# Optimization experiments

Hardware: AMD Instinct MI355X
Metric: run time of the kernel (lower is better)

Reference implementation:

```python
import jax, jax.numpy as jnp
import numpy as np

B, T, N, H, MAX_LAG = 16, 28, 2048, 32, 7
LN_EPS = 1e-5


def setup_inputs() -> dict:
    key = jax.random.key(0)
    ks = jax.random.split(key, 10)
    s = 1.0 / np.sqrt(H)  # nn.Linear-like init scale
    x = jax.random.uniform(ks[0], (B, T, N), dtype=jnp.float32)
    features = jax.random.normal(ks[1], (B, N, H), dtype=jnp.float32)
    # delay logits init: log(softmax-able exp(-tau/3) normalized + 1e-8)
    w = np.exp(-np.arange(MAX_LAG + 1, dtype=np.float32) / 3.0)
    w = w / w.sum()
    delay_logits = jnp.log(jnp.asarray(w, dtype=jnp.float32) + 1e-8)
    Wq = jax.random.normal(ks[2], (H, H), dtype=jnp.float32) * s
    Wk = jax.random.normal(ks[3], (H, H), dtype=jnp.float32) * s
    Wv = jax.random.normal(ks[4], (H, H), dtype=jnp.float32) * s
    Wo = jax.random.normal(ks[5], (H, H), dtype=jnp.float32) * s
    bq = jnp.zeros((H,), jnp.float32)
    bk = jnp.zeros((H,), jnp.float32)
    bv = jnp.zeros((H,), jnp.float32)
    bo = jnp.zeros((H,), jnp.float32)
    adj = jax.random.uniform(ks[6], (N, N), dtype=jnp.float32)
    adj_prior = adj / (adj.sum(axis=-1, keepdims=True) + 1e-8)  # row-normalized
    geo_weight = jnp.float32(0.3)
    gamma = jnp.ones((H,), jnp.float32)
    beta = jnp.zeros((H,), jnp.float32)
    return {"x": x, "features": features, "delay_logits": delay_logits,
            "Wq": Wq, "bq": bq, "Wk": Wk, "bk": bk, "Wv": Wv, "bv": bv,
            "adj_prior": adj_prior, "geo_weight": geo_weight,
            "Wo": Wo, "bo": bo, "gamma": gamma, "beta": beta}


def reference(x, features, delay_logits, Wq, bq, Wk, bk, Wv, bv,
              adj_prior, geo_weight, Wo, bo, gamma, beta):
    L = MAX_LAG + 1  # number of delay taps (T >= L here)
    delay_w = jax.nn.softmax(delay_logits, axis=0)  # [L]
    # delayed signal: sum_tau w[tau] * x[:, -(tau+1), :]
    lagged = x[:, -L:, :][:, ::-1, :]               # [B, L, N], tau-th row = x[:, -(tau+1)]
    delayed_signal = jnp.einsum('t,btn->bn', delay_w, lagged)  # [B, N]

    Q = features @ Wq.T + bq                        # [B, N, H]
    K = features @ Wk.T + bk
    V = features @ Wv.T + bv
    scores = jnp.einsum('bnh,bmh->bnm', Q, K) / np.sqrt(H).astype(np.float32)
    geo = jax.nn.sigmoid(geo_weight)
    scores = (1.0 - geo) * scores + geo * adj_prior[None, :, :] * 5.0
    attn = jax.nn.softmax(scores, axis=-1)          # [B, N, N]

    propagated = jnp.einsum('bnm,bm->bn', attn, delayed_signal)  # [B, N]
    attended = jnp.einsum('bnm,bmh->bnh', attn, V)               # [B, N, H]
    combined = features + attended + propagated[..., None] * 0.1

    h = combined @ Wo.T + bo
    mu = h.mean(axis=-1, keepdims=True)
    var = ((h - mu) ** 2).mean(axis=-1, keepdims=True)
    out = (h - mu) * jax.lax.rsqrt(var + LN_EPS) * gamma + beta
    return out
```

## Files before the change

kernel.cpp:

```cpp
#include <hip/hip_runtime.h>
#include <hip/hip_bf16.h>
#include <math.h>
#include <stdint.h>

#define Bb 16
#define Tt 28
#define Nn 2048
#define Hh 32
#define LAGS 8
#define LN_EPS 1e-5f
#define PSTR 56

typedef float f4 __attribute__((ext_vector_type(4)));
typedef short s8v __attribute__((ext_vector_type(8)));
typedef unsigned short u16x4 __attribute__((ext_vector_type(4)));
typedef unsigned short u16x8 __attribute__((ext_vector_type(8)));

__device__ __forceinline__ float b2f(unsigned short u) {
    union { unsigned uu; float ff; } x; x.uu = ((unsigned)u) << 16; return x.ff;
}
__device__ __forceinline__ unsigned short f2b(float f) {
    unsigned u = __float_as_uint(f);
    u += 0x7FFFu + ((u >> 16) & 1u);
    return (unsigned short)(u >> 16);
}
__device__ __forceinline__ unsigned packbf2(float lo, float hi) {
    __hip_bfloat162 h = __float22bfloat162_rn(make_float2(lo, hi));
    union { __hip_bfloat162 h2; unsigned u; } c; c.h2 = h; return c.u;
}

__global__ void k_adjprep(const float* __restrict__ adj, const float* __restrict__ geo_w,
                          unsigned short* __restrict__ adjF) {
    __shared__ float T[16][516];
    float geo = 1.f / (1.f + __expf(-geo_w[0]));
    float cg = geo * 5.f;
    int tid = threadIdx.x;
    int g = blockIdx.x >> 2, q = blockIdx.x & 3;
    int n0 = g * 16, m0 = q * 512;
    #pragma unroll
    for (int r = 0; r < 16; ++r) {
        T[r][tid] = adj[(size_t)(n0 + r) * Nn + m0 + tid];
        T[r][tid + 256] = adj[(size_t)(n0 + r) * Nn + m0 + tid + 256];
    }
    __syncthreads();
    unsigned short* region = adjF + ((size_t)g * 512 + q * 128) * 64;
    #pragma unroll
    for (int i = 0; i < 4; ++i) {
        int e0 = (i * 256 + tid) * 8;
        u16x8 w;
        #pragma unroll
        for (int j = 0; j < 8; ++j) {
            int e = e0 + j;
            int mq = e >> 6, nl = (e >> 2) & 15, mm = e & 3;
            w[j] = f2b(cg * T[nl][mq * 4 + mm]);
        }
        *(u16x8*)(region + e0) = w;
    }
}

__global__ void k_qkv(const float* __restrict__ feat, const float* __restrict__ x,
                      const float* __restrict__ dlog,
                      const float* __restrict__ Wq, const float* __restrict__ bq,
                      const float* __restrict__ Wk, const float* __restrict__ bk,
                      const float* __restrict__ Wv, const float* __restrict__ bv,
                      const float* __restrict__ geo_w,
                      unsigned short* __restrict__ Qbf, unsigned short* __restrict__ Kf,
                      unsigned short* __restrict__ Vf) {
    __shared__ float WqT[Hh][Hh + 1], WkT[Hh][Hh + 1], WvT[Hh][Hh + 1];
    __shared__ float f[8][Hh];
    __shared__ __align__(16) unsigned short VT8[Hh][8];
    __shared__ __align__(16) unsigned short DS8[8];
    int tid = threadIdx.x;
    for (int i = tid; i < Hh * Hh; i += 256) {
        int h = i >> 5, k = i & 31;
        WqT[k][h] = Wq[i];
        WkT[k][h] = Wk[i];
        WvT[k][h] = Wv[i];
    }
    int n0 = blockIdx.x * 8;
    int b = n0 >> 11, mloc0 = n0 & 2047;
    if (tid < 64) {
        float mx = -1e30f;
        #pragma unroll
        for (int t = 0; t < LAGS; ++t) mx = fmaxf(mx, dlog[t]);
        float s = 0.f, wv[LAGS];
        #pragma unroll
        for (int t = 0; t < LAGS; ++t) { wv[t] = __expf(dlog[t] - mx); s += wv[t]; }
        int t = tid >> 3, j = tid & 7;
        float dsv = (wv[t] / s) * x[(size_t)b * Tt * Nn + (size_t)(Tt - 1 - t) * Nn + mloc0 + j];
        dsv += __shfl_xor(dsv, 8);
        dsv += __shfl_xor(dsv, 16);
        dsv += __shfl_xor(dsv, 32);
        if (tid < 8) DS8[tid] = f2b(dsv);
    }
    float geo = 1.f / (1.f + __expf(-geo_w[0]));
    float cs = (1.f - geo) * 0.17677669529663687f;
    f[tid >> 5][tid & 31] = feat[(size_t)n0 * Hh + tid];
    __syncthreads();
    int lr = tid >> 5, h = tid & 31;
    float aq = bq[h], ak = bk[h], av = bv[h];
    #pragma unroll
    for (int k = 0; k < Hh; ++k) {
        float fv = f[lr][k];
        aq += fv * WqT[k][h];
        ak += fv * WkT[k][h];
        av += fv * WvT[k][h];
    }
    Qbf[(size_t)(n0 + lr) * Hh + h] = f2b(aq * cs);
    int mloc = mloc0 + lr;
    size_t kaddr = ((((size_t)b * 128 + (mloc >> 4)) * 4 + (h >> 3)) * 16 + (mloc & 15)) * 8 + (h & 7);
    Kf[kaddr] = f2b(ak);
    VT8[h][lr] = f2b(av);
    __syncthreads();
    size_t vbase = (((size_t)b * 64 + (mloc0 >> 5)) * 4 + ((mloc0 >> 3) & 3)) * 48;
    if (tid < 32) {
        *(u16x8*)(Vf + (vbase + tid) * 8) = *(const u16x8*)&VT8[tid][0];
    } else if (tid < 48) {
        int rr = tid - 32;
        u16x8 wv8;
        if (rr == 0) {
            wv8 = *(const u16x8*)&DS8[0];
        } else {
            unsigned short fill = (rr == 1) ? (unsigned short)0x3F80 : (unsigned short)0;
            for (int j = 0; j < 8; ++j) wv8[j] = fill;
        }
        *(u16x8*)(Vf + (vbase + 32 + rr) * 8) = wv8;
    }
}

__global__ __launch_bounds__(256, 2)
void k_attn(const unsigned short* __restrict__ Qbf,
            const unsigned short* __restrict__ Kf,
            const unsigned short* __restrict__ Vf,
            const unsigned short* __restrict__ adjF,
            const float* __restrict__ feat,
            const float* __restrict__ Wo, const float* __restrict__ bo,
            const float* __restrict__ gamma, const float* __restrict__ beta,
            float* __restrict__ out) {
    __shared__ __align__(16) unsigned short Pt[4][32 * PSTR];
    __shared__ float WoT[Hh][Hh + 1];
    __shared__ float combT[32][Hh + 1];
    __shared__ float gbb[3][Hh];

    int tid = threadIdx.x;
    int wid = tid >> 6, lane = tid & 63;
    int nl = lane & 15, g4 = lane >> 4;
    int wh = wid;

    for (int i = tid; i < Hh * Hh; i += 256) WoT[i & 31][i >> 5] = Wo[i];
    if (tid < 32) { gbb[0][tid] = bo[tid]; gbb[1][tid] = gamma[tid]; gbb[2][tid] = beta[tid]; }

    int bid = blockIdx.x;
    int xcd = bid & 7, r = bid >> 3;
    int b = ((xcd & 1) << 3) + (r & 7);
    int nt32 = ((xcd >> 1) << 4) + (r >> 3);
    int n0w = nt32 * 32;

    s8v qf[2];
    #pragma unroll
    for (int nt = 0; nt < 2; ++nt)
        qf[nt] = *(const s8v*)(Qbf + (((size_t)b * Nn + n0w + nt * 16 + nl) << 5) + g4 * 8);

    f4 pacc[2][3];
    #pragma unroll
    for (int nt = 0; nt < 2; ++nt)
        #pragma unroll
        for (int t = 0; t < 3; ++t) pacc[nt][t] = (f4){0.f, 0.f, 0.f, 0.f};

    const unsigned short* Kb = Kf + (size_t)b * 65536;
    const unsigned short* Vb = Vf + (size_t)b * 98304;
    unsigned short* Pw = Pt[wid];

    const unsigned short* pK  = Kb + (((size_t)(wh * 2) * 4 + g4) * 16 + nl) * 8;
    const unsigned short* pV  = Vb + (((size_t)wh * 4 + g4) * 48 + nl) * 8;
    const unsigned short* pA0 = adjF + ((size_t)(nt32 * 2) * 512 + wh * 8 + g4) * 64 + nl * 4;
    const unsigned short* pA1 = adjF + ((size_t)(nt32 * 2 + 1) * 512 + wh * 8 + g4) * 64 + nl * 4;

    struct Frag {
        s8v kf0, kf1, vf0, vf1, vf2;
        u16x4 a00, a01, a10, a11;
    };

    auto loadP = [&](Frag& F) {
        F.kf0 = *(const s8v*)(pK);
        F.kf1 = *(const s8v*)(pK + 512);
        F.vf0 = *(const s8v*)(pV);
        F.vf1 = *(const s8v*)(pV + 128);
        F.vf2 = *(const s8v*)(pV + 256);
        F.a00 = *(const u16x4*)(pA0);
        F.a01 = *(const u16x4*)(pA0 + 256);
        F.a10 = *(const u16x4*)(pA1);
        F.a11 = *(const u16x4*)(pA1 + 256);
        pK += 4096;
        pV += 6144;
        pA0 += 2048;
        pA1 += 2048;
    };

    auto mkC = [&](u16x4 av) -> f4 {
        f4 C;
        C[0] = b2f(av[0]); C[1] = b2f(av[1]); C[2] = b2f(av[2]); C[3] = b2f(av[3]);
        return C;
    };

    auto SM = [&](f4 sc, int nt, int mg) {
        float p0 = __expf(sc[0]), p1 = __expf(sc[1]);
        float p2 = __expf(sc[2]), p3 = __expf(sc[3]);
        uint2 w;
        w.x = packbf2(p0, p1);
        w.y = packbf2(p2, p3);
        *(uint2*)(Pw + (size_t)(nt * 16 + nl) * PSTR + mg * 16 + g4 * 4) = w;
    };

    auto compute = [&](Frag& F) {
        f4 sc00 = __builtin_amdgcn_mfma_f32_16x16x32_bf16(F.kf0, qf[0], mkC(F.a00), 0, 0, 0);
        f4 sc01 = __builtin_amdgcn_mfma_f32_16x16x32_bf16(F.kf1, qf[0], mkC(F.a01), 0, 0, 0);
        f4 sc10 = __builtin_amdgcn_mfma_f32_16x16x32_bf16(F.kf0, qf[1], mkC(F.a10), 0, 0, 0);
        f4 sc11 = __builtin_amdgcn_mfma_f32_16x16x32_bf16(F.kf1, qf[1], mkC(F.a11), 0, 0, 0);
        SM(sc00, 0, 0);
        SM(sc01, 0, 1);
        SM(sc10, 1, 0);
        SM(sc11, 1, 1);
        s8v pb0 = *(const s8v*)(Pw + (size_t)(0 * 16 + nl) * PSTR + g4 * 8);
        s8v pb1 = *(const s8v*)(Pw + (size_t)(1 * 16 + nl) * PSTR + g4 * 8);
        pacc[0][0] = __builtin_amdgcn_mfma_f32_16x16x32_bf16(F.vf0, pb0, pacc[0][0], 0, 0, 0);
        pacc[0][1] = __builtin_amdgcn_mfma_f32_16x16x32_bf16(F.vf1, pb0, pacc[0][1], 0, 0, 0);
        pacc[0][2] = __builtin_amdgcn_mfma_f32_16x16x32_bf16(F.vf2, pb0, pacc[0][2], 0, 0, 0);
        pacc[1][0] = __builtin_amdgcn_mfma_f32_16x16x32_bf16(F.vf0, pb1, pacc[1][0], 0, 0, 0);
        pacc[1][1] = __builtin_amdgcn_mfma_f32_16x16x32_bf16(F.vf1, pb1, pacc[1][1], 0, 0, 0);
        pacc[1][2] = __builtin_amdgcn_mfma_f32_16x16x32_bf16(F.vf2, pb1, pacc[1][2], 0, 0, 0);
    };

    const int NC = Nn / 128;
    Frag A, B;
    loadP(A);
    for (int c = 0; c < NC; c += 2) {
        loadP(B);
        compute(A);
        if (c + 2 < NC) loadP(A);
        compute(B);
    }

    float* mrgb = (float*)&Pt[0][0];
    __syncthreads();
    if (wh & 1) {
        float* d = mrgb + ((size_t)(wh >> 1) * 64 + lane) * 24;
        #pragma unroll
        for (int nt = 0; nt < 2; ++nt)
            #pragma unroll
            for (int t = 0; t < 3; ++t)
                #pragma unroll
                for (int r2 = 0; r2 < 4; ++r2) d[(nt * 3 + t) * 4 + r2] = pacc[nt][t][r2];
    }
    __syncthreads();
    if (!(wh & 1)) {
        const float* d = mrgb + ((size_t)(wh >> 1) * 64 + lane) * 24;
        #pragma unroll
        for (int nt = 0; nt < 2; ++nt)
            #pragma unroll
            for (int t = 0; t < 3; ++t)
                #pragma unroll
                for (int r2 = 0; r2 < 4; ++r2) pacc[nt][t][r2] += d[(nt * 3 + t) * 4 + r2];
    }
    __syncthreads();
    if (wh == 2) {
        float* d = mrgb + (size_t)lane * 24;
        #pragma unroll
        for (int nt = 0; nt < 2; ++nt)
            #pragma unroll
            for (int t = 0; t < 3; ++t)
                #pragma unroll
                for (int r2 = 0; r2 < 4; ++r2) d[(nt * 3 + t) * 4 + r2] = pacc[nt][t][r2];
    }
    __syncthreads();
    if (wh == 0) {
        const float* d = mrgb + (size_t)lane * 24;
        #pragma unroll
        for (int nt = 0; nt < 2; ++nt)
            #pragma unroll
            for (int t = 0; t < 3; ++t)
                #pragma unroll
                for (int r2 = 0; r2 < 4; ++r2) pacc[nt][t][r2] += d[(nt * 3 + t) * 4 + r2];

        #pragma unroll
        for (int nt = 0; nt < 2; ++nt) {
            float psn = __shfl(pacc[nt][2][1], nl);
            float prn = __shfl(pacc[nt][2][0], nl);
            float invS = 1.f / psn;
            float pp = prn * invS * 0.1f;
            size_t o = ((size_t)b * Nn + n0w + nt * 16 + nl) * Hh;
            #pragma unroll
            for (int t = 0; t < 2; ++t) {
                f4 fv = *(const f4*)(feat + o + t * 16 + g4 * 4);
                #pragma unroll
                for (int r2 = 0; r2 < 4; ++r2)
                    combT[nt * 16 + nl][t * 16 + g4 * 4 + r2] = fv[r2] + pacc[nt][t][r2] * invS + pp;
            }
        }
    }
    __syncthreads();

    int h = lane & 31;
    #pragma unroll
    for (int pass = 0; pass < 4; ++pass) {
        int row = wh * 8 + pass * 2 + (lane >> 5);
        float a = gbb[0][h];
        #pragma unroll
        for (int k = 0; k < Hh; ++k) a += combT[row][k] * WoT[k][h];
        float mu = a;
        #pragma unroll
        for (int w = 1; w < 32; w <<= 1) mu += __shfl_xor(mu, w);
        mu *= (1.f / 32.f);
        float dd = a - mu;
        float v = dd * dd;
        #pragma unroll
        for (int w = 1; w < 32; w <<= 1) v += __shfl_xor(v, w);
        v *= (1.f / 32.f);
        out[((size_t)b * Nn + n0w + row) * Hh + h] =
            dd * rsqrtf(v + LN_EPS) * gbb[1][h] + gbb[2][h];
    }
}

extern "C" void kernel_launch(void* const* d_in, const int* in_sizes, int n_in,
                              void* d_out, int out_size, void* d_ws, size_t ws_size,
                              hipStream_t stream) {
    const float* x     = (const float*)d_in[0];
    const float* feat  = (const float*)d_in[1];
    const float* dlog  = (const float*)d_in[2];
    const float* Wq    = (const float*)d_in[3];
    const float* bq    = (const float*)d_in[4];
    const float* Wk    = (const float*)d_in[5];
    const float* bk    = (const float*)d_in[6];
    const float* Wv    = (const float*)d_in[7];
    const float* bv    = (const float*)d_in[8];
    const float* adj   = (const float*)d_in[9];
    const float* geo   = (const float*)d_in[10];
    const float* Wo    = (const float*)d_in[11];
    const float* bo    = (const float*)d_in[12];
    const float* gamma = (const float*)d_in[13];
    const float* beta  = (const float*)d_in[14];
    float* out = (float*)d_out;

    char* w = (char*)d_ws;
    unsigned short* Qbf  = (unsigned short*)w;  w += (size_t)Bb * Nn * Hh * 2;
    unsigned short* Kf   = (unsigned short*)w;  w += (size_t)Bb * Nn * Hh * 2;
    unsigned short* Vf   = (unsigned short*)w;  w += (size_t)Bb * 98304 * 2;
    unsigned short* adjF = (unsigned short*)w;  w += (size_t)Nn * Nn * 2;

    k_adjprep<<<512, 256, 0, stream>>>(adj, geo, adjF);
    k_qkv<<<Bb * Nn / 8, 256, 0, stream>>>(feat, x, dlog, Wq, bq, Wk, bk, Wv, bv, geo,
                                           Qbf, Kf, Vf);
    k_attn<<<1024, 256, 0, stream>>>(Qbf, Kf, Vf, adjF, feat, Wo, bo, gamma, beta, out);
}
```

Baseline: 53.96 us.

## Software-pipeline QK softmax and PV MFMA stages with double-buffered P tiles

Splits the per-chunk attention step into a QK^T+exp stage that writes P to LDS and a PV MFMA stage, then skews them across iterations with two P buffers per wave. The PV matmul for one chunk now runs alongside the score computation of the next, hiding the LDS write-then-read latency and the exp work behind MFMA. This doubles the per-wave P LDS footprint, which could reduce occupancy, and adds register pressure from carrying V fragments across stages.

After: 53.62 us. About the same (-0.6%).

```diff
diff --git a/kernel.cpp b/kernel.cpp
--- a/kernel.cpp
+++ b/kernel.cpp
@@ -137,7 +137,7 @@
             const float* __restrict__ Wo, const float* __restrict__ bo,
             const float* __restrict__ gamma, const float* __restrict__ beta,
             float* __restrict__ out) {
-    __shared__ __align__(16) unsigned short Pt[4][32 * PSTR];
+    __shared__ __align__(16) unsigned short Pt[4][2][32 * PSTR];
     __shared__ float WoT[Hh][Hh + 1];
     __shared__ float combT[32][Hh + 1];
     __shared__ float gbb[3][Hh];
@@ -169,7 +169,8 @@
 
     const unsigned short* Kb = Kf + (size_t)b * 65536;
     const unsigned short* Vb = Vf + (size_t)b * 98304;
-    unsigned short* Pw = Pt[wid];
+    unsigned short* Pw0 = Pt[wid][0];
+    unsigned short* Pw1 = Pt[wid][1];
 
     const unsigned short* pK  = Kb + (((size_t)(wh * 2) * 4 + g4) * 16 + nl) * 8;
     const unsigned short* pV  = Vb + (((size_t)wh * 4 + g4) * 48 + nl) * 8;
@@ -203,7 +204,7 @@
         return C;
     };
 
-    auto SM = [&](f4 sc, int nt, int mg) {
+    auto SM = [&](f4 sc, int nt, int mg, unsigned short* Pw) {
         float p0 = __expf(sc[0]), p1 = __expf(sc[1]);
         float p2 = __expf(sc[2]), p3 = __expf(sc[3]);
         uint2 w;
@@ -212,36 +213,60 @@
         *(uint2*)(Pw + (size_t)(nt * 16 + nl) * PSTR + mg * 16 + g4 * 4) = w;
     };
 
-    auto compute = [&](Frag& F) {
+    auto qks = [&](Frag& F, unsigned short* Pw) {
         f4 sc00 = __builtin_amdgcn_mfma_f32_16x16x32_bf16(F.kf0, qf[0], mkC(F.a00), 0, 0, 0);
         f4 sc01 = __builtin_amdgcn_mfma_f32_16x16x32_bf16(F.kf1, qf[0], mkC(F.a01), 0, 0, 0);
         f4 sc10 = __builtin_amdgcn_mfma_f32_16x16x32_bf16(F.kf0, qf[1], mkC(F.a10), 0, 0, 0);
         f4 sc11 = __builtin_amdgcn_mfma_f32_16x16x32_bf16(F.kf1, qf[1], mkC(F.a11), 0, 0, 0);
-        SM(sc00, 0, 0);
-        SM(sc01, 0, 1);
-        SM(sc10, 1, 0);
-        SM(sc11, 1, 1);
-        s8v pb0 = *(const s8v*)(Pw + (size_t)(0 * 16 + nl) * PSTR + g4 * 8);
-        s8v pb1 = *(const s8v*)(Pw + (size_t)(1 * 16 + nl) * PSTR + g4 * 8);
-        pacc[0][0] = __builtin_amdgcn_mfma_f32_16x16x32_bf16(F.vf0, pb0, pacc[0][0], 0, 0, 0);
-        pacc[0][1] = __builtin_amdgcn_mfma_f32_16x16x32_bf16(F.vf1, pb0, pacc[0][1], 0, 0, 0);
-        pacc[0][2] = __builtin_amdgcn_mfma_f32_16x16x32_bf16(F.vf2, pb0, pacc[0][2], 0, 0, 0);
-        pacc[1][0] = __builtin_amdgcn_mfma_f32_16x16x32_bf16(F.vf0, pb1, pacc[1][0], 0, 0, 0);
-        pacc[1][1] = __builtin_amdgcn_mfma_f32_16x16x32_bf16(F.vf1, pb1, pacc[1][1], 0, 0, 0);
-        pacc[1][2] = __builtin_amdgcn_mfma_f32_16x16x32_bf16(F.vf2, pb1, pacc[1][2], 0, 0, 0);
+        SM(sc00, 0, 0, Pw);
+        SM(sc01, 0, 1, Pw);
+        SM(sc10, 1, 0, Pw);
+        SM(sc11, 1, 1, Pw);
+    };
+
+    auto readP = [&](const unsigned short* Pw, s8v& pb0, s8v& pb1) {
+        pb0 = *(const s8v*)(Pw + (size_t)(0 * 16 + nl) * PSTR + g4 * 8);
+        pb1 = *(const s8v*)(Pw + (size_t)(1 * 16 + nl) * PSTR + g4 * 8);
+    };
+
+    auto pvm = [&](s8v v0, s8v v1, s8v v2, s8v pb0, s8v pb1) {
+        pacc[0][0] = __builtin_amdgcn_mfma_f32_16x16x32_bf16(v0, pb0, pacc[0][0], 0, 0, 0);
+        pacc[0][1] = __builtin_amdgcn_mfma_f32_16x16x32_bf16(v1, pb0, pacc[0][1], 0, 0, 0);
+        pacc[0][2] = __builtin_amdgcn_mfma_f32_16x16x32_bf16(v2, pb0, pacc[0][2], 0, 0, 0);
+        pacc[1][0] = __builtin_amdgcn_mfma_f32_16x16x32_bf16(v0, pb1, pacc[1][0], 0, 0, 0);
+        pacc[1][1] = __builtin_amdgcn_mfma_f32_16x16x32_bf16(v1, pb1, pacc[1][1], 0, 0, 0);
+        pacc[1][2] = __builtin_amdgcn_mfma_f32_16x16x32_bf16(v2, pb1, pacc[1][2], 0, 0, 0);
     };
 
     const int NC = Nn / 128;
     Frag A, B;
+    s8v sv0, sv1, sv2, pb0, pb1;
+
     loadP(A);
-    for (int c = 0; c < NC; c += 2) {
+    loadP(B);
+    qks(A, Pw0);
+    sv0 = A.vf0; sv1 = A.vf1; sv2 = A.vf2;
+
+    for (int i = 0; i < (NC - 2) / 2; ++i) {
+        readP(Pw0, pb0, pb1);
+        loadP(A);
+        qks(B, Pw1);
+        pvm(sv0, sv1, sv2, pb0, pb1);
+        sv0 = B.vf0; sv1 = B.vf1; sv2 = B.vf2;
         loadP(B);
-        compute(A);
-        if (c + 2 < NC) loadP(A);
-        compute(B);
-    }
-
-    float* mrgb = (float*)&Pt[0][0];
+        readP(Pw1, pb0, pb1);
+        qks(A, Pw0);
+        pvm(sv0, sv1, sv2, pb0, pb1);
+        sv0 = A.vf0; sv1 = A.vf1; sv2 = A.vf2;
+    }
+    readP(Pw0, pb0, pb1);
+    qks(B, Pw1);
+    pvm(sv0, sv1, sv2, pb0, pb1);
+    sv0 = B.vf0; sv1 = B.vf1; sv2 = B.vf2;
+    readP(Pw1, pb0, pb1);
+    pvm(sv0, sv1, sv2, pb0, pb1);
+
+    float* mrgb = (float*)&Pt[0][0][0];
     __syncthreads();
     if (wh & 1) {
         float* d = mrgb + ((size_t)(wh >> 1) * 64 + lane) * 24;
```
